# Kernel optimization log

Hardware: AMD Instinct MI355X
Metric: run time of the kernel (lower is better)

Reference implementation:

```python
import jax, jax.numpy as jnp
import numpy as np

B, S, D = 1, 8192, 768
T_MAX = 1000.0  # timestamp range (days); keeps beta*tau <= 1 so exp is well-behaved


def setup_inputs() -> dict:
    key = jax.random.key(0)
    k1, k2 = jax.random.split(key)
    h = jax.random.normal(k1, (B, S, D), dtype=jnp.float32)
    # timestamps: sorted ascending per timeline (posts arrive in time order)
    t = jnp.sort(jax.random.uniform(k2, (B, S), dtype=jnp.float32) * T_MAX, axis=-1)
    # learned scalar parameters of HeatLayer
    epsilon = jnp.asarray(0.01, dtype=jnp.float32)
    beta = jnp.asarray(0.001, dtype=jnp.float32)
    return {"h": h, "t": t, "epsilon": epsilon, "beta": beta}


def reference(h, t, epsilon, beta):
    """HEAT layer: out[b,i] = sum_{j: t[i]>=t[j]} h[b,j] + relu(h[b,j]) * eps * exp(beta*(t[i]-t[j])).

    Matches apply_heat_on_matrix_representations with temporal_direction='past',
    exclude_current_post=False, sum_decay_with_original=True,
    allow_negative_decay=False, background_intensity='default', no padding.
    """
    tau = t[:, :, None] - t[:, None, :]            # [B,S,S] pairwise time deltas
    mask = (tau >= 0).astype(h.dtype)              # causal (past incl. current) mask
    W = epsilon * jnp.exp(beta * tau) * mask       # Hawkes decay weights
    out = jnp.einsum('bij,bjd->bid', mask, h) \
        + jnp.einsum('bij,bjd->bid', W, jnp.maximum(h, 0.0))
    return out
```

## Files before the change

### kernel.cpp

```cpp
#include <hip/hip_runtime.h>


namespace {
constexpr int S   = 8192;
constexpr int D   = 768;
constexpr int DV  = D / 4;
constexpr int CH  = 64;
constexpr int NC  = S / CH;
constexpr int QL  = 32;
constexpr int NG  = DV / QL;
constexpr int RG  = 8;
constexpr int RR  = CH / RG;
constexpr int SEG = 16;
constexpr int CPS = NC / SEG;
constexpr int QPB = 16;
constexpr int SBP = DV / QPB;
}

typedef float f4raw __attribute__((ext_vector_type(4)));

__device__ __forceinline__ float4 f4add(float4 a, float4 b) {
    return make_float4(a.x + b.x, a.y + b.y, a.z + b.z, a.w + b.w);
}
__device__ __forceinline__ void f4relu_fma(float4& acc, float4 h, float d) {
    acc.x += fmaxf(h.x, 0.f) * d;
    acc.y += fmaxf(h.y, 0.f) * d;
    acc.z += fmaxf(h.z, 0.f) * d;
    acc.w += fmaxf(h.w, 0.f) * d;
}

__global__ __launch_bounds__(256)
void heat_partials(const float* __restrict__ h, const float* __restrict__ t,
                   const float* __restrict__ betap,
                   float4* __restrict__ SP1, float4* __restrict__ SQ1) {
    const int tid = threadIdx.x, lane = tid & (QL - 1), r = tid / QL;
    const int c = blockIdx.x, g = blockIdx.y;
    const int q = g * QL + lane;
    __shared__ float dec[CH];
    __shared__ float4 rgP[RG][QL], rgQ[RG][QL];
    const float4* h4 = (const float4*)h;
    const int row0 = c * CH + r * RR;
    float4 hv[RR];
#pragma unroll
    for (int k = 0; k < RR; ++k) hv[k] = h4[(size_t)(row0 + k) * DV + q];
    if (tid < CH) dec[tid] = expf(-betap[0] * t[c * CH + tid]);
    __syncthreads();
    float4 pp = {0, 0, 0, 0}, qq = {0, 0, 0, 0};
#pragma unroll
    for (int k = 0; k < RR; ++k) {
        pp = f4add(pp, hv[k]);
        f4relu_fma(qq, hv[k], dec[r * RR + k]);
    }
    rgP[r][lane] = pp;
    rgQ[r][lane] = qq;
    __syncthreads();
    if (r == 0) {
        float4 sp = rgP[0][lane];
#pragma unroll
        for (int w = 1; w < RG; ++w) sp = f4add(sp, rgP[w][lane]);
        SP1[c * DV + q] = sp;
    } else if (r == 1) {
        float4 sq = rgQ[0][lane];
#pragma unroll
        for (int w = 1; w < RG; ++w) sq = f4add(sq, rgQ[w][lane]);
        SQ1[c * DV + q] = sq;
    }
}

__global__ __launch_bounds__(256)
void heat_scan(const float4* __restrict__ SP1, const float4* __restrict__ SQ1,
               float4* __restrict__ offP, float4* __restrict__ offQ) {
    const int blk = blockIdx.x;
    const bool isQ = blk >= SBP;
    const int lb = isQ ? blk - SBP : blk;
    const float4* src = isQ ? SQ1 : SP1;
    float4*       dst = isQ ? offQ : offP;
    const int qk = threadIdx.x & (QPB - 1);
    const int sg = threadIdx.x >> 4;
    const int qs = lb * QPB + qk;
    const int c0 = sg * CPS;
    __shared__ float4 ssum[SEG][QPB];
    float4 v[CPS];
#pragma unroll
    for (int u = 0; u < CPS; ++u) v[u] = src[(c0 + u) * DV + qs];
    float4 tot = {0, 0, 0, 0};
#pragma unroll
    for (int u = 0; u < CPS; ++u) tot = f4add(tot, v[u]);
    ssum[sg][qk] = tot;
    __syncthreads();
    float4 run = {0, 0, 0, 0};
    for (int s2 = 0; s2 < SEG - 1; ++s2)
        if (s2 < sg) run = f4add(run, ssum[s2][qk]);
#pragma unroll
    for (int u = 0; u < CPS; ++u) {
        dst[(c0 + u) * DV + qs] = run;
        run = f4add(run, v[u]);
    }
}

__global__ __launch_bounds__(256)
void heat_out(const float* __restrict__ h, const float* __restrict__ t,
              const float* __restrict__ epsp, const float* __restrict__ betap,
              const float4* __restrict__ offP, const float4* __restrict__ offQ,
              float* __restrict__ out) {
    const int tid  = threadIdx.x;
    const int lane = tid & (QL - 1);
    const int r    = tid / QL;
    const int c    = blockIdx.x;
    const int g    = blockIdx.y;
    const int q    = g * QL + lane;
    const float eps = epsp[0], beta = betap[0];

    __shared__ float tt[CH + 1];
    __shared__ float dec[CH], epv[CH];
    __shared__ float4 rgP[RG][QL], rgQ[RG][QL];

    const float4* h4   = (const float4*)h;
    float4*       out4 = (float4*)out;
    const int row0 = c * CH + r * RR;

    float4 hv[RR];
#pragma unroll
    for (int k = 0; k < RR; ++k) hv[k] = h4[(size_t)(row0 + k) * DV + q];
    float4 po = offP[(size_t)c * DV + q];
    float4 qo = offQ[(size_t)c * DV + q];

    if (tid <= CH) {
        int j = c * CH + tid;
        tt[tid] = (j < S) ? t[j] : 1e30f;
    }
    __syncthreads();
    if (tid < CH) {
        float tv = tt[tid];
        dec[tid] = expf(-beta * tv);
        epv[tid] = eps * expf(beta * tv);
    }
    __syncthreads();

    const float4 z = {0, 0, 0, 0};
    float4 pp = z, qq = z;
#pragma unroll
    for (int k = 0; k < RR; ++k) {
        pp = f4add(pp, hv[k]);
        f4relu_fma(qq, hv[k], dec[r * RR + k]);
    }
    rgP[r][lane] = pp;
    rgQ[r][lane] = qq;
    __syncthreads();

#pragma unroll
    for (int rr2 = 0; rr2 < RG - 1; ++rr2)
        if (rr2 < r) {
            po = f4add(po, rgP[rr2][lane]);
            qo = f4add(qo, rgQ[rr2][lane]);
        }

#pragma unroll
    for (int k = 0; k < RR; ++k) {
        po = f4add(po, hv[k]);
        f4relu_fma(qo, hv[k], dec[r * RR + k]);
        const float ep = epv[r * RR + k];
        float4 o;
        o.x = po.x + ep * qo.x;
        o.y = po.y + ep * qo.y;
        o.z = po.z + ep * qo.z;
        o.w = po.w + ep * qo.w;
        const int lr = r * RR + k;
        if (tt[lr + 1] == tt[lr]) {
            int j = row0 + k + 1;
            const float tcur = tt[lr];
            float tj = tt[lr + 1];
            while (tj == tcur) {
                float4 hj = h4[(size_t)j * DV + q];
                o.x += hj.x + eps * fmaxf(hj.x, 0.f);
                o.y += hj.y + eps * fmaxf(hj.y, 0.f);
                o.z += hj.z + eps * fmaxf(hj.z, 0.f);
                o.w += hj.w + eps * fmaxf(hj.w, 0.f);
                ++j;
                if (j >= S) break;
                const int lj = j - c * CH;
                tj = (lj <= CH) ? tt[lj] : t[j];
            }
        }
        __builtin_nontemporal_store(*(const f4raw*)&o,
            (f4raw*)(out4 + (size_t)(row0 + k) * DV + q));
    }
}

extern "C" void kernel_launch(void* const* d_in, const int* in_sizes, int n_in,
                              void* d_out, int out_size, void* d_ws, size_t ws_size,
                              hipStream_t stream) {
    const float* h    = (const float*)d_in[0];
    const float* t    = (const float*)d_in[1];
    const float* eps  = (const float*)d_in[2];
    const float* beta = (const float*)d_in[3];
    float* out = (float*)d_out;

    float4* SP1  = (float4*)d_ws;
    float4* SQ1  = SP1 + (size_t)NC * DV;
    float4* offP = SQ1 + (size_t)NC * DV;
    float4* offQ = offP + (size_t)NC * DV;

    heat_partials<<<dim3(NC, NG), 256, 0, stream>>>(h, t, beta, SP1, SQ1);
    heat_scan<<<2 * SBP, 256, 0, stream>>>(SP1, SQ1, offP, offQ);
    heat_out<<<dim3(NC, NG), 256, 0, stream>>>(h, t, eps, beta, offP, offQ, out);
}
```

Before: 19.60 us.

## Drop separate scan kernel; compute chunk prefix offsets inside output kernel

Removes the middle scan launch. Each output block now sums all preceding chunk partials itself, spread across its 8 row groups and reduced in shared memory. The chunk size doubles to 128 so there are fewer partials to sum. This saves one kernel launch and the offset write/read round trip, but adds redundant, quadratic-in-chunk-count partial reads for later chunks and halves the grid size.

```diff
diff --git a/kernel.cpp b/kernel.cpp
--- a/kernel.cpp
+++ b/kernel.cpp
@@ -5,16 +5,12 @@
 constexpr int S   = 8192;
 constexpr int D   = 768;
 constexpr int DV  = D / 4;
-constexpr int CH  = 64;
+constexpr int CH  = 128;
 constexpr int NC  = S / CH;
 constexpr int QL  = 32;
 constexpr int NG  = DV / QL;
 constexpr int RG  = 8;
 constexpr int RR  = CH / RG;
-constexpr int SEG = 16;
-constexpr int CPS = NC / SEG;
-constexpr int QPB = 16;
-constexpr int SBP = DV / QPB;
 }
 
 typedef float f4raw __attribute__((ext_vector_type(4)));
@@ -68,40 +64,9 @@
 }
 
 __global__ __launch_bounds__(256)
-void heat_scan(const float4* __restrict__ SP1, const float4* __restrict__ SQ1,
-               float4* __restrict__ offP, float4* __restrict__ offQ) {
-    const int blk = blockIdx.x;
-    const bool isQ = blk >= SBP;
-    const int lb = isQ ? blk - SBP : blk;
-    const float4* src = isQ ? SQ1 : SP1;
-    float4*       dst = isQ ? offQ : offP;
-    const int qk = threadIdx.x & (QPB - 1);
-    const int sg = threadIdx.x >> 4;
-    const int qs = lb * QPB + qk;
-    const int c0 = sg * CPS;
-    __shared__ float4 ssum[SEG][QPB];
-    float4 v[CPS];
-#pragma unroll
-    for (int u = 0; u < CPS; ++u) v[u] = src[(c0 + u) * DV + qs];
-    float4 tot = {0, 0, 0, 0};
-#pragma unroll
-    for (int u = 0; u < CPS; ++u) tot = f4add(tot, v[u]);
-    ssum[sg][qk] = tot;
-    __syncthreads();
-    float4 run = {0, 0, 0, 0};
-    for (int s2 = 0; s2 < SEG - 1; ++s2)
-        if (s2 < sg) run = f4add(run, ssum[s2][qk]);
-#pragma unroll
-    for (int u = 0; u < CPS; ++u) {
-        dst[(c0 + u) * DV + qs] = run;
-        run = f4add(run, v[u]);
-    }
-}
-
-__global__ __launch_bounds__(256)
 void heat_out(const float* __restrict__ h, const float* __restrict__ t,
               const float* __restrict__ epsp, const float* __restrict__ betap,
-              const float4* __restrict__ offP, const float4* __restrict__ offQ,
+              const float4* __restrict__ SP1, const float4* __restrict__ SQ1,
               float* __restrict__ out) {
     const int tid  = threadIdx.x;
     const int lane = tid & (QL - 1);
@@ -114,6 +79,7 @@
     __shared__ float tt[CH + 1];
     __shared__ float dec[CH], epv[CH];
     __shared__ float4 rgP[RG][QL], rgQ[RG][QL];
+    __shared__ float4 redP[RG][QL], redQ[RG][QL];
 
     const float4* h4   = (const float4*)h;
     float4*       out4 = (float4*)out;
@@ -122,8 +88,17 @@
     float4 hv[RR];
 #pragma unroll
     for (int k = 0; k < RR; ++k) hv[k] = h4[(size_t)(row0 + k) * DV + q];
-    float4 po = offP[(size_t)c * DV + q];
-    float4 qo = offQ[(size_t)c * DV + q];
+
+    const float4 z = {0, 0, 0, 0};
+    float4 aP = z, aQ = z;
+#pragma unroll
+    for (int u = 0; u < NC / RG; ++u) {
+        const int p = r + RG * u;
+        if (p < c) {
+            aP = f4add(aP, SP1[(size_t)p * DV + q]);
+            aQ = f4add(aQ, SQ1[(size_t)p * DV + q]);
+        }
+    }
 
     if (tid <= CH) {
         int j = c * CH + tid;
@@ -137,7 +112,6 @@
     }
     __syncthreads();
 
-    const float4 z = {0, 0, 0, 0};
     float4 pp = z, qq = z;
 #pragma unroll
     for (int k = 0; k < RR; ++k) {
@@ -146,8 +120,16 @@
     }
     rgP[r][lane] = pp;
     rgQ[r][lane] = qq;
+    redP[r][lane] = aP;
+    redQ[r][lane] = aQ;
     __syncthreads();
 
+    float4 po = redP[0][lane], qo = redQ[0][lane];
+#pragma unroll
+    for (int w = 1; w < RG; ++w) {
+        po = f4add(po, redP[w][lane]);
+        qo = f4add(qo, redQ[w][lane]);
+    }
 #pragma unroll
     for (int rr2 = 0; rr2 < RG - 1; ++rr2)
         if (rr2 < r) {
@@ -196,12 +178,9 @@
     const float* beta = (const float*)d_in[3];
     float* out = (float*)d_out;
 
-    float4* SP1  = (float4*)d_ws;
-    float4* SQ1  = SP1 + (size_t)NC * DV;
-    float4* offP = SQ1 + (size_t)NC * DV;
-    float4* offQ = offP + (size_t)NC * DV;
+    float4* SP1 = (float4*)d_ws;
+    float4* SQ1 = SP1 + (size_t)NC * DV;
 
     heat_partials<<<dim3(NC, NG), 256, 0, stream>>>(h, t, beta, SP1, SQ1);
-    heat_scan<<<2 * SBP, 256, 0, stream>>>(SP1, SQ1, offP, offQ);
-    heat_out<<<dim3(NC, NG), 256, 0, stream>>>(h, t, eps, beta, offP, offQ, out);
+    heat_out<<<dim3(NC, NG), 256, 0, stream>>>(h, t, eps, beta, SP1, SQ1, out);
 }
```

After: 20.63 us. 5.2% more time.
